# Optimization experiments

Hardware: AMD Instinct MI355X
Metric: run time of the kernel (lower is better)

Reference implementation:

```python
import jax, jax.numpy as jnp
import numpy as np

N_HEADS = 16
BLOCK_SIZE = 256


def setup_inputs() -> dict:
    key = jax.random.key(0)
    ks = jax.random.split(key, 5)
    B, T, C = 4, 4096, 1024
    scale = 0.02
    return {
        "x": jax.random.normal(ks[0], (B, T, C), dtype=jnp.float32),
        "Wqkv": jax.random.normal(ks[1], (C, 3 * C), dtype=jnp.float32) * scale,
        "bqkv": jnp.zeros((3 * C,), dtype=jnp.float32),
        "Wout": jax.random.normal(ks[2], (C, C), dtype=jnp.float32) * scale,
        "bout": jnp.zeros((C,), dtype=jnp.float32),
    }


def reference(x, Wqkv, bqkv, Wout, bout):
    B, T, C = x.shape
    H = N_HEADS
    hd = C // H
    bs = BLOCK_SIZE
    nb = T // bs

    qkv = x @ Wqkv + bqkv                     # [B,T,3C]
    qkv = qkv.reshape(B, T, H, 3 * hd).transpose(0, 2, 1, 3)  # [B,H,T,3hd]
    q, k, v = jnp.split(qkv, 3, axis=-1)      # each [B,H,T,hd]

    # block-diagonal local attention: reshape T -> (nb, bs)
    q = q.reshape(B, H, nb, bs, hd)
    k = k.reshape(B, H, nb, bs, hd)
    v = v.reshape(B, H, nb, bs, hd)

    scores = jnp.einsum("bhnqd,bhnkd->bhnqk", q, k) * (hd ** -0.5)
    attn = jax.nn.softmax(scores, axis=-1)
    o = jnp.einsum("bhnqk,bhnkd->bhnqd", attn, v)  # [B,H,nb,bs,hd]

    o = o.reshape(B, H, T, hd).transpose(0, 2, 1, 3).reshape(B, T, C)
    return o @ Wout + bout
```

## Files before the change

kernel.cpp:

```cpp
#include <hip/hip_runtime.h>

typedef unsigned int u32;
typedef unsigned short u16;
typedef short bf16x8 __attribute__((ext_vector_type(8)));
typedef u16 u16x8 __attribute__((ext_vector_type(8)));
typedef float f32x4 __attribute__((ext_vector_type(4)));


__device__ __forceinline__ u16 f2bf(float f) {
  unsigned u = __float_as_uint(f);
  u += 0x7FFFu + ((u >> 16) & 1u);
  return (u16)(u >> 16);
}

typedef const void __attribute__((address_space(1)))* gas_p;
typedef void __attribute__((address_space(3)))* las_p;

__device__ __forceinline__ void async_ld16(const void* g, void* l) {
  __builtin_amdgcn_global_load_lds((gas_p)g, (las_p)l, 16, 0, 0);
}


__global__ __launch_bounds__(256) void k_cvt_bf16(const float* __restrict__ in,
                                                  u16* __restrict__ out, int n8) {
  int i = blockIdx.x * 256 + threadIdx.x;
  if (i >= n8) return;
  const float4* p = (const float4*)in + (size_t)i * 2;
  float4 a = p[0], b = p[1];
  u16x8 o;
  o[0] = f2bf(a.x); o[1] = f2bf(a.y); o[2] = f2bf(a.z); o[3] = f2bf(a.w);
  o[4] = f2bf(b.x); o[5] = f2bf(b.y); o[6] = f2bf(b.z); o[7] = f2bf(b.w);
  *((u16x8*)out + i) = o;
}


__global__ __launch_bounds__(256) void k_transpose_cvt(const float* __restrict__ in,
                                                       u16* __restrict__ out,
                                                       int R, int Ncols) {
  __shared__ u16 t[32][33];
  int tx = threadIdx.x, ty = threadIdx.y;
  int c0 = blockIdx.x * 32, r0 = blockIdx.y * 32;
#pragma unroll
  for (int j = 0; j < 32; j += 8)
    t[ty + j][tx] = f2bf(in[(size_t)(r0 + ty + j) * Ncols + c0 + tx]);
  __syncthreads();
#pragma unroll
  for (int j = 0; j < 32; j += 8)
    out[(size_t)(c0 + ty + j) * R + r0 + tx] = t[tx][ty + j];
}


#define MFMA2(m, n)                                                                   \
  acc[m][n] = __builtin_amdgcn_mfma_f32_16x16x32_bf16(a[m][0], b[n][0], acc[m][n], 0, 0, 0); \
  acc[m][n] = __builtin_amdgcn_mfma_f32_16x16x32_bf16(a[m][1], b[n][1], acc[m][n], 0, 0, 0);

#define STAGE_A(h_, T_, dd_) do {                                          \
    const u16* g_ = pAg + (size_t)(h_) * 128 * KK + (size_t)(T_) * 64;     \
    u16* s_ = lds + (dd_) * 16384 + ((h_) * 128 + w * 16) * 64;            \
    async_ld16(g_, s_);                                                    \
    async_ld16(g_ + 8 * (size_t)KK, s_ + 512);                             \
  } while (0)

#define STAGE_B(h_, T_, dd_) do {                                          \
    const u16* g_ = pBg + (size_t)(h_) * 128 * KK + (size_t)(T_) * 64;     \
    u16* s_ = lds + 32768 + (dd_) * 16384 + ((h_) * 128 + w * 16) * 64;    \
    async_ld16(g_, s_);                                                    \
    async_ld16(g_ + 8 * (size_t)KK, s_ + 512);                             \
  } while (0)

#define TB(k_, d_)                                                              \
  {                                                                             \
    const int doA = (d_) * 16384, doB = 32768 + (d_) * 16384;                   \
    _Pragma("unroll") for (int f = 0; f < 4; ++f) {                             \
      a[f][0] = *(const bf16x8*)(lds + doA + rAoff + f * 1024 + c0);            \
      a[f][1] = *(const bf16x8*)(lds + doA + rAoff + f * 1024 + c1);            \
    }                                                                           \
    _Pragma("unroll") for (int f = 0; f < 2; ++f) {                             \
      b[f][0] = *(const bf16x8*)(lds + doB + rBoff + f * 1024 + c0);            \
      b[f][1] = *(const bf16x8*)(lds + doB + rBoff + f * 1024 + c1);            \
    }                                                                           \
    if ((k_) + 1 < NT) STAGE_B(0, (k_) + 1, (d_) ^ 1);                          \
    asm volatile("s_waitcnt lgkmcnt(8)");                                       \
    __builtin_amdgcn_s_barrier();                                               \
    asm volatile("s_waitcnt lgkmcnt(0)");                                       \
    __builtin_amdgcn_s_setprio(1);                                              \
    MFMA2(0, 0); MFMA2(1, 0); MFMA2(2, 0); MFMA2(3, 0);                         \
    MFMA2(0, 1); MFMA2(1, 1); MFMA2(2, 1); MFMA2(3, 1);                         \
    __builtin_amdgcn_s_setprio(0);                                              \
    __builtin_amdgcn_s_barrier();                                               \
    _Pragma("unroll") for (int f = 4; f < 8; ++f) {                             \
      a[f][0] = *(const bf16x8*)(lds + doA + rAoff + f * 1024 + c0);            \
      a[f][1] = *(const bf16x8*)(lds + doA + rAoff + f * 1024 + c1);            \
    }                                                                           \
    if ((k_) + 1 < NT) STAGE_B(1, (k_) + 1, (d_) ^ 1);                          \
    __builtin_amdgcn_s_barrier();                                               \
    asm volatile("s_waitcnt lgkmcnt(0)");                                       \
    __builtin_amdgcn_s_setprio(1);                                              \
    MFMA2(4, 0); MFMA2(5, 0); MFMA2(6, 0); MFMA2(7, 0);                         \
    MFMA2(4, 1); MFMA2(5, 1); MFMA2(6, 1); MFMA2(7, 1);                         \
    __builtin_amdgcn_s_setprio(0);                                              \
    __builtin_amdgcn_s_barrier();                                               \
    _Pragma("unroll") for (int f = 2; f < 4; ++f) {                             \
      b[f][0] = *(const bf16x8*)(lds + doB + rBoff + f * 1024 + c0);            \
      b[f][1] = *(const bf16x8*)(lds + doB + rBoff + f * 1024 + c1);            \
    }                                                                           \
    if ((k_) + 2 < NT) STAGE_A(0, (k_) + 2, (d_));                              \
    __builtin_amdgcn_s_barrier();                                               \
    asm volatile("s_waitcnt lgkmcnt(0)");                                       \
    __builtin_amdgcn_s_setprio(1);                                              \
    MFMA2(4, 2); MFMA2(5, 2); MFMA2(6, 2); MFMA2(7, 2);                         \
    MFMA2(4, 3); MFMA2(5, 3); MFMA2(6, 3); MFMA2(7, 3);                         \
    __builtin_amdgcn_s_setprio(0);                                              \
    __builtin_amdgcn_s_barrier();                                               \
    if ((k_) + 2 < NT) STAGE_A(1, (k_) + 2, (d_));                              \
    __builtin_amdgcn_s_setprio(1);                                              \
    MFMA2(0, 2); MFMA2(1, 2); MFMA2(2, 2); MFMA2(3, 2);                         \
    MFMA2(0, 3); MFMA2(1, 3); MFMA2(2, 3); MFMA2(3, 3);                         \
    __builtin_amdgcn_s_setprio(0);                                              \
    if ((k_) < NT - 2) { asm volatile("s_waitcnt vmcnt(4)"); }                  \
    else               { asm volatile("s_waitcnt vmcnt(0)"); }                  \
    __builtin_amdgcn_s_barrier();                                               \
  }

#define EPI(PM0, PN0) do {                                                      \
    int ccol0 = (PN0) + wn * 64 + (lane & 15);                                  \
    float bv0 = bias[ccol0], bv1 = bias[ccol0 + 16];                            \
    float bv2 = bias[ccol0 + 32], bv3 = bias[ccol0 + 48];                       \
    size_t crow0 = (size_t)((PM0) + wm * 128 + ((lane >> 4) << 2));             \
    _Pragma("unroll") for (int m = 0; m < 8; ++m)                               \
    _Pragma("unroll") for (int reg = 0; reg < 4; ++reg) {                       \
      size_t ro = (crow0 + m * 16 + reg) * (size_t)N + ccol0;                   \
      float v0 = acc[m][0][reg] + bv0, v1 = acc[m][1][reg] + bv1;               \
      float v2 = acc[m][2][reg] + bv2, v3 = acc[m][3][reg] + bv3;               \
      if (OUT_BF16) {                                                           \
        ((u16*)Cout)[ro] = f2bf(v0); ((u16*)Cout)[ro + 16] = f2bf(v1);          \
        ((u16*)Cout)[ro + 32] = f2bf(v2); ((u16*)Cout)[ro + 48] = f2bf(v3);     \
      } else {                                                                  \
        ((float*)Cout)[ro] = v0; ((float*)Cout)[ro + 16] = v1;                  \
        ((float*)Cout)[ro + 32] = v2; ((float*)Cout)[ro + 48] = v3;             \
      }                                                                         \
    }                                                                           \
  } while (0)

template <int OUT_BF16, int KK>
__global__ __launch_bounds__(512, 2) void k_gemm8(const u16* __restrict__ A,
                                                  const u16* __restrict__ Bt,
                                                  const float* __restrict__ bias,
                                                  void* __restrict__ Cout,
                                                  int M, int N) {
  extern __shared__ u16 lds[];
  const int NT = KK / 64;

  int nbn = N >> 8, nbm = M >> 8, nwg = nbm * nbn;
  int tid = threadIdx.x;
  int w = tid >> 6, lane = tid & 63;
  int wm = w >> 2, wn = w & 3;

  int rAoff = (wm * 128 + (lane & 15)) << 6;
  int rBoff = (wn * 64 + (lane & 15)) << 6;
  int hi8 = (lane >> 4) << 3, key8 = (lane & 7) << 3;
  int c0 = hi8 ^ key8;
  int c1 = (32 | hi8) ^ key8;
  int rowoff = w * 16 + (lane >> 3);
  int soff = ((lane & 7) ^ (lane >> 3)) << 3;

  bf16x8 a[8][2], b[4][2];
  f32x4 acc[8][4];
  const u16 *pAg = A, *pBg = Bt;
  int pm0 = 0, pn0 = 0;

  for (int t = blockIdx.x; t < nwg; t += gridDim.x) {
    int q = nwg >> 3, r = nwg & 7, x = t & 7, loc = t >> 3;
    int swz = (x < r ? x * (q + 1) : r * (q + 1) + (x - r) * q) + loc;
    int mi = swz / nbn, ni = swz % nbn;
    int m0 = mi << 8, n0 = ni << 8;

    if (t != (int)blockIdx.x) EPI(pm0, pn0);

    pAg = A + (size_t)(m0 + rowoff) * KK + soff;
    pBg = Bt + (size_t)(n0 + rowoff) * KK + soff;
    STAGE_A(0, 0, 0); STAGE_A(1, 0, 0); STAGE_B(0, 0, 0); STAGE_B(1, 0, 0);
    STAGE_A(0, 1, 1); STAGE_A(1, 1, 1);
    asm volatile("s_waitcnt vmcnt(4)");
    __builtin_amdgcn_s_barrier();

#pragma unroll
    for (int m = 0; m < 8; ++m)
#pragma unroll
      for (int n = 0; n < 4; ++n) acc[m][n] = (f32x4){0.f, 0.f, 0.f, 0.f};

    for (int k = 0; k < NT; k += 2) {
      TB(k, 0);
      TB(k + 1, 1);
    }
    pm0 = m0; pn0 = n0;
  }
  EPI(pm0, pn0);
}


__global__ __launch_bounds__(512, 2) void k_attn2(const u16* __restrict__ qkv,
                                                  u16* __restrict__ o) {
  __shared__ u16 ldsK[256 * 64];
  __shared__ u16 ldsV[64 * 256];

  int bid = blockIdx.x;
  int g = ((bid & 7) << 7) | (bid >> 3);
  int blk = g & 15, h = (g >> 4) & 15, b = g >> 8;

  int tid = threadIdx.x;
  int w = tid >> 6, lane = tid & 63;
  int hgrp = lane >> 4;
  size_t rowb = ((size_t)(b * 4096 + blk * 256)) * 3072 + (size_t)h * 192;

  int qbase = w * 32;
  const u16* qp0 = qkv + rowb + (size_t)(qbase + (lane & 15)) * 3072 + hgrp * 8;
  const u16* qp1 = qp0 + (size_t)16 * 3072;
  bf16x8 qf00 = *(const bf16x8*)(qp0);
  bf16x8 qf01 = *(const bf16x8*)(qp0 + 32);
  bf16x8 qf10 = *(const bf16x8*)(qp1);
  bf16x8 qf11 = *(const bf16x8*)(qp1 + 32);

#pragma unroll
  for (int it = 0; it < 4; ++it) {
    int trow = it * 64 + (tid >> 3);
    const u16* ksrc = qkv + rowb + (size_t)trow * 3072 + 64 +
                      (((lane & 7) ^ (lane >> 3)) << 3);
    async_ld16(ksrc, ldsK + (it * 64 + w * 8) * 64);
    int d0 = (tid & 7) << 3;
    uint4 vv = *(const uint4*)(qkv + rowb + (size_t)trow * 3072 + 128 + d0);
    union { uint4 v; u16 s[8]; } uv;
    uv.v = vv;
#pragma unroll
    for (int j = 0; j < 8; ++j) {
      int d = d0 + j;
      int key = (((d & 7) ^ ((d >> 3) & 7)) & 7) << 4;
      *(u16*)((char*)ldsV + d * 512 + ((2 * trow) ^ key)) = uv.s[j];
    }
  }
  __syncthreads();

  f32x4 acc0[16] = {}, acc1[16] = {};
  int cb = hgrp << 4;
#pragma unroll
  for (int ct = 0; ct < 16; ++ct) {
    int krow = ct * 16 + (lane & 15);
    const char* kb = (const char*)ldsK + krow * 128;
    int key = (krow & 7) << 4;
    bf16x8 k0 = *(const bf16x8*)(kb + (cb ^ key));
    bf16x8 k1 = *(const bf16x8*)(kb + ((64 + cb) ^ key));
    acc0[ct] = __builtin_amdgcn_mfma_f32_16x16x32_bf16(k0, qf00, acc0[ct], 0, 0, 0);
    acc0[ct] = __builtin_amdgcn_mfma_f32_16x16x32_bf16(k1, qf01, acc0[ct], 0, 0, 0);
    acc1[ct] = __builtin_amdgcn_mfma_f32_16x16x32_bf16(k0, qf10, acc1[ct], 0, 0, 0);
    acc1[ct] = __builtin_amdgcn_mfma_f32_16x16x32_bf16(k1, qf11, acc1[ct], 0, 0, 0);
  }

  const float SC = 0.125f * 1.44269504f;
  float rden0, rden1;
  {
    float mx = -1e30f;
#pragma unroll
    for (int ct = 0; ct < 16; ++ct)
#pragma unroll
      for (int rg = 0; rg < 4; ++rg) mx = fmaxf(mx, acc0[ct][rg]);
    mx = fmaxf(mx, __shfl_xor(mx, 16));
    mx = fmaxf(mx, __shfl_xor(mx, 32));
    float s = 0.f;
#pragma unroll
    for (int ct = 0; ct < 16; ++ct)
#pragma unroll
      for (int rg = 0; rg < 4; ++rg) {
        float p = exp2f((acc0[ct][rg] - mx) * SC);
        acc0[ct][rg] = p;
        s += p;
      }
    s += __shfl_xor(s, 16);
    s += __shfl_xor(s, 32);
    rden0 = 1.f / s;
  }
  {
    float mx = -1e30f;
#pragma unroll
    for (int ct = 0; ct < 16; ++ct)
#pragma unroll
      for (int rg = 0; rg < 4; ++rg) mx = fmaxf(mx, acc1[ct][rg]);
    mx = fmaxf(mx, __shfl_xor(mx, 16));
    mx = fmaxf(mx, __shfl_xor(mx, 32));
    float s = 0.f;
#pragma unroll
    for (int ct = 0; ct < 16; ++ct)
#pragma unroll
      for (int rg = 0; rg < 4; ++rg) {
        float p = exp2f((acc1[ct][rg] - mx) * SC);
        acc1[ct][rg] = p;
        s += p;
      }
    s += __shfl_xor(s, 16);
    s += __shfl_xor(s, 32);
    rden1 = 1.f / s;
  }

  int s1 = (lane & 15) + ((lane >> 4) & 1) * 32;
  int s2 = s1 + 16;
  bool lo = (lane < 32);
  bf16x8 pa0[8], pa1[8];
#define PCONV(ACC, PA)                                                      \
  _Pragma("unroll") for (int kt = 0; kt < 8; ++kt) {                        \
    u32 wA0, wB0, wA1, wB1;                                                 \
    asm("v_cvt_pk_bf16_f32 %0, %1, %2" : "=v"(wA0)                          \
        : "v"(ACC[2 * kt][0]), "v"(ACC[2 * kt][1]));                        \
    asm("v_cvt_pk_bf16_f32 %0, %1, %2" : "=v"(wB0)                          \
        : "v"(ACC[2 * kt][2]), "v"(ACC[2 * kt][3]));                        \
    asm("v_cvt_pk_bf16_f32 %0, %1, %2" : "=v"(wA1)                          \
        : "v"(ACC[2 * kt + 1][0]), "v"(ACC[2 * kt + 1][1]));                \
    asm("v_cvt_pk_bf16_f32 %0, %1, %2" : "=v"(wB1)                          \
        : "v"(ACC[2 * kt + 1][2]), "v"(ACC[2 * kt + 1][3]));                \
    u32 t0a = (u32)__shfl((int)wA0, s1), t0b = (u32)__shfl((int)wA1, s1);   \
    u32 t1a = (u32)__shfl((int)wB0, s1), t1b = (u32)__shfl((int)wB1, s1);   \
    u32 t2a = (u32)__shfl((int)wA0, s2), t2b = (u32)__shfl((int)wA1, s2);   \
    u32 t3a = (u32)__shfl((int)wB0, s2), t3b = (u32)__shfl((int)wB1, s2);   \
    union { u32 w[4]; bf16x8 v; } pu;                                       \
    pu.w[0] = lo ? t0a : t0b;                                               \
    pu.w[1] = lo ? t1a : t1b;                                               \
    pu.w[2] = lo ? t2a : t2b;                                               \
    pu.w[3] = lo ? t3a : t3b;                                               \
    PA[kt] = pu.v;                                                          \
  }
  PCONV(acc0, pa0)
  PCONV(acc1, pa1)
#undef PCONV

  f32x4 oa0[4] = {}, oa1[4] = {};
#pragma unroll
  for (int kt = 0; kt < 8; ++kt) {
    int vkb = 2 * (kt * 32 + hgrp * 8);
#pragma unroll
    for (int nt = 0; nt < 4; ++nt) {
      int vd = nt * 16 + (lane & 15);
      int key = (((vd & 7) ^ ((vd >> 3) & 7)) & 7) << 4;
      bf16x8 vf = *(const bf16x8*)((char*)ldsV + vd * 512 + (vkb ^ key));
      oa0[nt] = __builtin_amdgcn_mfma_f32_16x16x32_bf16(pa0[kt], vf, oa0[nt], 0, 0, 0);
      oa1[nt] = __builtin_amdgcn_mfma_f32_16x16x32_bf16(pa1[kt], vf, oa1[nt], 0, 0, 0);
    }
  }

  float rd0[4], rd1[4];
#pragma unroll
  for (int rg = 0; rg < 4; ++rg) {
    rd0[rg] = __shfl(rden0, 4 * hgrp + rg, 16);
    rd1[rg] = __shfl(rden1, 4 * hgrp + rg, 16);
  }
  size_t ob = ((size_t)(b * 4096 + blk * 256 + qbase)) * 1024 + (size_t)h * 64;
#pragma unroll
  for (int nt = 0; nt < 4; ++nt)
#pragma unroll
    for (int rg = 0; rg < 4; ++rg) {
      int col = nt * 16 + (lane & 15);
      o[ob + (size_t)(4 * hgrp + rg) * 1024 + col] = f2bf(oa0[nt][rg] * rd0[rg]);
      o[ob + (size_t)(16 + 4 * hgrp + rg) * 1024 + col] = f2bf(oa1[nt][rg] * rd1[rg]);
    }
}


extern "C" void kernel_launch(void* const* d_in, const int* in_sizes, int n_in,
                              void* d_out, int out_size, void* d_ws, size_t ws_size,
                              hipStream_t stream) {
  (void)in_sizes; (void)n_in; (void)out_size; (void)ws_size;
  const float* x = (const float*)d_in[0];
  const float* Wqkv = (const float*)d_in[1];
  const float* bqkv = (const float*)d_in[2];
  const float* Wout = (const float*)d_in[3];
  const float* bout = (const float*)d_in[4];
  float* out = (float*)d_out;

  char* ws = (char*)d_ws;
  u16* xb    = (u16*)(ws + 0);
  u16* wqkvT = (u16*)(ws + 33554432);
  u16* woT   = (u16*)(ws + 39845888);
  u16* qkv   = (u16*)(ws + 41943040);
  u16* ob    = (u16*)(ws + 142606336);

  hipFuncSetAttribute(reinterpret_cast<const void*>(&k_gemm8<1, 1024>),
                      hipFuncAttributeMaxDynamicSharedMemorySize, 131072);
  hipFuncSetAttribute(reinterpret_cast<const void*>(&k_gemm8<0, 1024>),
                      hipFuncAttributeMaxDynamicSharedMemorySize, 131072);

  k_cvt_bf16<<<8192, 256, 0, stream>>>(x, xb, 16384 * 1024 / 8);
  k_transpose_cvt<<<dim3(96, 32), dim3(32, 8), 0, stream>>>(Wqkv, wqkvT, 1024, 3072);
  k_transpose_cvt<<<dim3(32, 32), dim3(32, 8), 0, stream>>>(Wout, woT, 1024, 1024);

  k_gemm8<1, 1024><<<256, 512, 131072, stream>>>(xb, wqkvT, bqkv, qkv, 16384, 3072);

  k_attn2<<<1024, 512, 0, stream>>>(qkv, ob);

  k_gemm8<0, 1024><<<256, 512, 131072, stream>>>(ob, woT, bout, out, 16384, 1024);
}
```

Baseline: 229.4 us.

## Prefetch next tile's operands during current tile's tail in persistent GEMM

New measurement: 228.5 us. About the same (-0.4%).

```diff
diff --git a/kernel.cpp b/kernel.cpp
--- a/kernel.cpp
+++ b/kernel.cpp
@@ -50,76 +50,74 @@
 }
 
 
-#define MFMA2(m, n)                                                                   \
-  acc[m][n] = __builtin_amdgcn_mfma_f32_16x16x32_bf16(a[m][0], b[n][0], acc[m][n], 0, 0, 0); \
-  acc[m][n] = __builtin_amdgcn_mfma_f32_16x16x32_bf16(a[m][1], b[n][1], acc[m][n], 0, 0, 0);
-
-#define STAGE_A(h_, T_, dd_) do {                                          \
-    const u16* g_ = pAg + (size_t)(h_) * 128 * KK + (size_t)(T_) * 64;     \
-    u16* s_ = lds + (dd_) * 16384 + ((h_) * 128 + w * 16) * 64;            \
+#define STAGE_A2(h_, src_, dd_) do {                                       \
+    const u16* g_ = (src_) + (size_t)(h_) * 128 * KK;                      \
+    u16* s_ = lds + (dd_) * 16384 + (((h_) * 128 + w * 16) << 6);          \
     async_ld16(g_, s_);                                                    \
     async_ld16(g_ + 8 * (size_t)KK, s_ + 512);                             \
   } while (0)
 
-#define STAGE_B(h_, T_, dd_) do {                                          \
-    const u16* g_ = pBg + (size_t)(h_) * 128 * KK + (size_t)(T_) * 64;     \
-    u16* s_ = lds + 32768 + (dd_) * 16384 + ((h_) * 128 + w * 16) * 64;    \
+#define STAGE_B2(h_, src_, dd_) do {                                       \
+    const u16* g_ = (src_) + (size_t)(h_) * 128 * KK;                      \
+    u16* s_ = lds + 32768 + (dd_) * 16384 + (((h_) * 128 + w * 16) << 6);  \
     async_ld16(g_, s_);                                                    \
     async_ld16(g_ + 8 * (size_t)KK, s_ + 512);                             \
   } while (0)
 
-#define TB(k_, d_)                                                              \
-  {                                                                             \
-    const int doA = (d_) * 16384, doB = 32768 + (d_) * 16384;                   \
-    _Pragma("unroll") for (int f = 0; f < 4; ++f) {                             \
-      a[f][0] = *(const bf16x8*)(lds + doA + rAoff + f * 1024 + c0);            \
-      a[f][1] = *(const bf16x8*)(lds + doA + rAoff + f * 1024 + c1);            \
-    }                                                                           \
-    _Pragma("unroll") for (int f = 0; f < 2; ++f) {                             \
-      b[f][0] = *(const bf16x8*)(lds + doB + rBoff + f * 1024 + c0);            \
-      b[f][1] = *(const bf16x8*)(lds + doB + rBoff + f * 1024 + c1);            \
-    }                                                                           \
-    if ((k_) + 1 < NT) STAGE_B(0, (k_) + 1, (d_) ^ 1);                          \
-    asm volatile("s_waitcnt lgkmcnt(8)");                                       \
-    __builtin_amdgcn_s_barrier();                                               \
-    asm volatile("s_waitcnt lgkmcnt(0)");                                       \
-    __builtin_amdgcn_s_setprio(1);                                              \
-    MFMA2(0, 0); MFMA2(1, 0); MFMA2(2, 0); MFMA2(3, 0);                         \
-    MFMA2(0, 1); MFMA2(1, 1); MFMA2(2, 1); MFMA2(3, 1);                         \
-    __builtin_amdgcn_s_setprio(0);                                              \
-    __builtin_amdgcn_s_barrier();                                               \
-    _Pragma("unroll") for (int f = 4; f < 8; ++f) {                             \
-      a[f][0] = *(const bf16x8*)(lds + doA + rAoff + f * 1024 + c0);            \
-      a[f][1] = *(const bf16x8*)(lds + doA + rAoff + f * 1024 + c1);            \
-    }                                                                           \
-    if ((k_) + 1 < NT) STAGE_B(1, (k_) + 1, (d_) ^ 1);                          \
-    __builtin_amdgcn_s_barrier();                                               \
-    asm volatile("s_waitcnt lgkmcnt(0)");                                       \
-    __builtin_amdgcn_s_setprio(1);                                              \
-    MFMA2(4, 0); MFMA2(5, 0); MFMA2(6, 0); MFMA2(7, 0);                         \
-    MFMA2(4, 1); MFMA2(5, 1); MFMA2(6, 1); MFMA2(7, 1);                         \
-    __builtin_amdgcn_s_setprio(0);                                              \
-    __builtin_amdgcn_s_barrier();                                               \
-    _Pragma("unroll") for (int f = 2; f < 4; ++f) {                             \
-      b[f][0] = *(const bf16x8*)(lds + doB + rBoff + f * 1024 + c0);            \
-      b[f][1] = *(const bf16x8*)(lds + doB + rBoff + f * 1024 + c1);            \
-    }                                                                           \
-    if ((k_) + 2 < NT) STAGE_A(0, (k_) + 2, (d_));                              \
-    __builtin_amdgcn_s_barrier();                                               \
-    asm volatile("s_waitcnt lgkmcnt(0)");                                       \
-    __builtin_amdgcn_s_setprio(1);                                              \
-    MFMA2(4, 2); MFMA2(5, 2); MFMA2(6, 2); MFMA2(7, 2);                         \
-    MFMA2(4, 3); MFMA2(5, 3); MFMA2(6, 3); MFMA2(7, 3);                         \
-    __builtin_amdgcn_s_setprio(0);                                              \
-    __builtin_amdgcn_s_barrier();                                               \
-    if ((k_) + 2 < NT) STAGE_A(1, (k_) + 2, (d_));                              \
-    __builtin_amdgcn_s_setprio(1);                                              \
-    MFMA2(0, 2); MFMA2(1, 2); MFMA2(2, 2); MFMA2(3, 2);                         \
-    MFMA2(0, 3); MFMA2(1, 3); MFMA2(2, 3); MFMA2(3, 3);                         \
-    __builtin_amdgcn_s_setprio(0);                                              \
-    if ((k_) < NT - 2) { asm volatile("s_waitcnt vmcnt(4)"); }                  \
-    else               { asm volatile("s_waitcnt vmcnt(0)"); }                  \
-    __builtin_amdgcn_s_barrier();                                               \
+#define MQUAD(M0, N0)                                                      \
+    _Pragma("unroll") for (int ks = 0; ks < 2; ++ks)                       \
+    _Pragma("unroll") for (int mm = 0; mm < 4; ++mm)                       \
+    _Pragma("unroll") for (int nn = 0; nn < 2; ++nn)                       \
+      acc[(M0) + mm][(N0) + nn] = __builtin_amdgcn_mfma_f32_16x16x32_bf16( \
+          a[(M0) + mm][ks], b[(N0) + nn][ks], acc[(M0) + mm][(N0) + nn], 0, 0, 0);
+
+#define TBX(d_, bS_, aS_)                                                  \
+  {                                                                        \
+    const int doA = (d_) * 16384, doB = 32768 + (d_) * 16384;              \
+    _Pragma("unroll") for (int f = 0; f < 4; ++f) {                        \
+      a[f][0] = *(const bf16x8*)(lds + doA + rAoff + f * 1024 + c0);       \
+      a[f][1] = *(const bf16x8*)(lds + doA + rAoff + f * 1024 + c1);       \
+    }                                                                      \
+    _Pragma("unroll") for (int f = 0; f < 2; ++f) {                        \
+      b[f][0] = *(const bf16x8*)(lds + doB + rBoff + f * 1024 + c0);       \
+      b[f][1] = *(const bf16x8*)(lds + doB + rBoff + f * 1024 + c1);       \
+    }                                                                      \
+    STAGE_B2(0, bS_, (d_) ^ 1);                                            \
+    asm volatile("s_waitcnt lgkmcnt(8)");                                  \
+    __builtin_amdgcn_s_barrier();                                          \
+    asm volatile("s_waitcnt lgkmcnt(0)");                                  \
+    __builtin_amdgcn_s_setprio(1);                                         \
+    MQUAD(0, 0)                                                            \
+    __builtin_amdgcn_s_setprio(0);                                         \
+    __builtin_amdgcn_s_barrier();                                          \
+    _Pragma("unroll") for (int f = 4; f < 8; ++f) {                        \
+      a[f][0] = *(const bf16x8*)(lds + doA + rAoff + f * 1024 + c0);       \
+      a[f][1] = *(const bf16x8*)(lds + doA + rAoff + f * 1024 + c1);       \
+    }                                                                      \
+    STAGE_B2(1, bS_, (d_) ^ 1);                                            \
+    __builtin_amdgcn_s_barrier();                                          \
+    asm volatile("s_waitcnt lgkmcnt(0)");                                  \
+    __builtin_amdgcn_s_setprio(1);                                         \
+    MQUAD(4, 0)                                                            \
+    __builtin_amdgcn_s_setprio(0);                                         \
+    __builtin_amdgcn_s_barrier();                                          \
+    _Pragma("unroll") for (int f = 2; f < 4; ++f) {                        \
+      b[f][0] = *(const bf16x8*)(lds + doB + rBoff + f * 1024 + c0);       \
+      b[f][1] = *(const bf16x8*)(lds + doB + rBoff + f * 1024 + c1);       \
+    }                                                                      \
+    STAGE_A2(0, aS_, (d_));                                                \
+    __builtin_amdgcn_s_barrier();                                          \
+    asm volatile("s_waitcnt lgkmcnt(0)");                                  \
+    __builtin_amdgcn_s_setprio(1);                                         \
+    MQUAD(4, 2)                                                            \
+    __builtin_amdgcn_s_setprio(0);                                         \
+    __builtin_amdgcn_s_barrier();                                          \
+    STAGE_A2(1, aS_, (d_));                                                \
+    __builtin_amdgcn_s_setprio(1);                                         \
+    MQUAD(0, 2)                                                            \
+    __builtin_amdgcn_s_setprio(0);                                         \
+    asm volatile("s_waitcnt vmcnt(4)");                                    \
+    __builtin_amdgcn_s_barrier();                                          \
   }
 
 #define EPI(PM0, PN0) do {                                                      \
@@ -142,6 +140,18 @@
     }                                                                           \
   } while (0)
 
+#define TILE_COORD(tt, mm0, nn0) do {                                           \
+    int q_ = nwg >> 3, r_ = nwg & 7, x_ = (tt) & 7, loc_ = (tt) >> 3;           \
+    int swz_ = (x_ < r_ ? x_ * (q_ + 1) : r_ * (q_ + 1) + (x_ - r_) * q_) + loc_;\
+    mm0 = (swz_ / nbn) << 8; nn0 = (swz_ % nbn) << 8;                           \
+  } while (0)
+
+#define ZERO_ACC do {                                                           \
+    _Pragma("unroll") for (int m = 0; m < 8; ++m)                               \
+    _Pragma("unroll") for (int n = 0; n < 4; ++n)                               \
+      acc[m][n] = (f32x4){0.f, 0.f, 0.f, 0.f};                                  \
+  } while (0)
+
 template <int OUT_BF16, int KK>
 __global__ __launch_bounds__(512, 2) void k_gemm8(const u16* __restrict__ A,
                                                   const u16* __restrict__ Bt,
@@ -166,36 +176,48 @@
 
   bf16x8 a[8][2], b[4][2];
   f32x4 acc[8][4];
-  const u16 *pAg = A, *pBg = Bt;
-  int pm0 = 0, pn0 = 0;
-
-  for (int t = blockIdx.x; t < nwg; t += gridDim.x) {
-    int q = nwg >> 3, r = nwg & 7, x = t & 7, loc = t >> 3;
-    int swz = (x < r ? x * (q + 1) : r * (q + 1) + (x - r) * q) + loc;
-    int mi = swz / nbn, ni = swz % nbn;
-    int m0 = mi << 8, n0 = ni << 8;
-
-    if (t != (int)blockIdx.x) EPI(pm0, pn0);
-
-    pAg = A + (size_t)(m0 + rowoff) * KK + soff;
-    pBg = Bt + (size_t)(n0 + rowoff) * KK + soff;
-    STAGE_A(0, 0, 0); STAGE_A(1, 0, 0); STAGE_B(0, 0, 0); STAGE_B(1, 0, 0);
-    STAGE_A(0, 1, 1); STAGE_A(1, 1, 1);
-    asm volatile("s_waitcnt vmcnt(4)");
-    __builtin_amdgcn_s_barrier();
-
-#pragma unroll
-    for (int m = 0; m < 8; ++m)
-#pragma unroll
-      for (int n = 0; n < 4; ++n) acc[m][n] = (f32x4){0.f, 0.f, 0.f, 0.f};
+
+  int t = blockIdx.x;
+  int m0, n0;
+  TILE_COORD(t, m0, n0);
+  const u16* pAg = A + (size_t)(m0 + rowoff) * KK + soff;
+  const u16* pBg = Bt + (size_t)(n0 + rowoff) * KK + soff;
+
+  STAGE_A2(0, pAg, 0); STAGE_A2(1, pAg, 0);
+  STAGE_B2(0, pBg, 0); STAGE_B2(1, pBg, 0);
+  STAGE_A2(0, pAg + 64, 1); STAGE_A2(1, pAg + 64, 1);
+  asm volatile("s_waitcnt vmcnt(4)");
+  __builtin_amdgcn_s_barrier();
+  ZERO_ACC;
+
+  for (;;) {
+    int tn = t + gridDim.x;
+    bool last = tn >= nwg;
+    const u16 *pAgN, *pBgN;
+    int m0N = m0, n0N = n0;
+    if (last) {
+      pAgN = pAg; pBgN = pBg;
+    } else {
+      TILE_COORD(tn, m0N, n0N);
+      pAgN = A + (size_t)(m0N + rowoff) * KK + soff;
+      pBgN = Bt + (size_t)(n0N + rowoff) * KK + soff;
+    }
 
     for (int k = 0; k < NT; k += 2) {
-      TB(k, 0);
-      TB(k + 1, 1);
+      const u16* bS1 = pBg + (k + 1) * 64;
+      const u16* aS2 = (k + 2 < NT) ? pAg + (k + 2) * 64 : pAgN + (k + 2 - NT) * 64;
+      TBX(0, bS1, aS2);
+      const u16* bS2 = (k + 2 < NT) ? pBg + (k + 2) * 64 : pBgN + (k + 2 - NT) * 64;
+      const u16* aS3 = (k + 3 < NT) ? pAg + (k + 3) * 64 : pAgN + (k + 3 - NT) * 64;
+      TBX(1, bS2, aS3);
     }
-    pm0 = m0; pn0 = n0;
-  }
-  EPI(pm0, pn0);
+
+    EPI(m0, n0);
+    if (last) break;
+    t = tn; m0 = m0N; n0 = n0N; pAg = pAgN; pBg = pBgN;
+    ZERO_ACC;
+  }
+  asm volatile("s_waitcnt vmcnt(0)");
 }
 
 
```
